# Kernel tuning notes

Hardware: AMD Instinct MI355X
Metric: run time of the kernel (lower is better)

## Reference

```python
import jax, jax.numpy as jnp
import numpy as np

N_NODES = 50000
N_EDGES = 800000
N_FEAT = 128
DIM = 64
N_GRAPHS = 512


def setup_inputs() -> dict:
    key = jax.random.key(0)
    k1, k2, k3, k4, k5, k6 = jax.random.split(key, 6)
    x = jax.random.normal(k1, (N_NODES, N_FEAT), dtype=jnp.float32)
    edge_index = jax.random.randint(k2, (2, N_EDGES), 0, N_NODES, dtype=jnp.int64)
    batch = jnp.sort(jax.random.randint(k3, (N_NODES,), 0, N_GRAPHS, dtype=jnp.int64))
    W1 = jax.random.normal(k4, (N_FEAT, DIM), dtype=jnp.float32) * 0.05
    W2 = jax.random.normal(k5, (DIM, DIM), dtype=jnp.float32) * 0.05
    Wfc = jax.random.normal(k6, (DIM, 1), dtype=jnp.float32) * 0.05
    return {"x": x, "edge_index": edge_index, "batch": batch,
            "W1": W1, "W2": W2, "Wfc": Wfc}


def _gcn_conv(h, src, dst, W):
    # GCNConv(normalize=False, bias=False): linear transform then scatter-add
    # over edges: out[dst] += (h @ W)[src]
    h = jnp.einsum('nf,fd->nd', h, W)
    return jax.ops.segment_sum(h[src], dst, num_segments=N_NODES)


def reference(x, edge_index, batch, W1, W2, Wfc):
    src, dst = edge_index[0], edge_index[1]
    h = jax.nn.relu(_gcn_conv(x, src, dst, W1))          # [N, DIM]
    h = _gcn_conv(h, src, dst, W2)                        # [N, DIM]
    # global_mean_pool over graph ids
    counts = jax.ops.segment_sum(jnp.ones((N_NODES,), h.dtype), batch,
                                 num_segments=N_GRAPHS)   # [G]
    pooled = jax.ops.segment_sum(h, batch, num_segments=N_GRAPHS)
    pooled = pooled / jnp.maximum(counts, 1.0)[:, None]   # [G, DIM]
    return jax.nn.sigmoid(pooled @ Wfc)                   # [G, 1]
```

## Files before the change

### kernel.cpp

```cpp
#include <hip/hip_runtime.h>
#include <cmath>

#define N_NODES 50000
#define N_EDGES 800000
#define N_FEAT 128
#define DIM 64
#define N_GRAPHS 512
#define GGRID ((N_NODES + 63) / 64)
#define NBKT GGRID
#define BH_BLK 128
#define EPB (N_EDGES / BH_BLK)
#define NCNT (NBKT * BH_BLK)
#define P2_NBLK ((NCNT + 511) / 512)
#define BKT_CAP 2048

__device__ __forceinline__ unsigned short f2bf(float f) {
  union { float f; unsigned int u; } v; v.f = f;
  return (unsigned short)((v.u + 0x7FFFu + ((v.u >> 16) & 1u)) >> 16);
}
__device__ __forceinline__ float bf2f(unsigned short u) {
  union { unsigned int u; float f; } v; v.u = (unsigned int)u << 16;
  return v.f;
}

__global__ __launch_bounds__(256) void bhist_w2fc(const int* __restrict__ dst,
                                                  int* __restrict__ cnt,
                                                  const float* __restrict__ W2,
                                                  const float* __restrict__ Wfc,
                                                  float* __restrict__ w2fc) {
  if (blockIdx.x == BH_BLK) {
    int k = threadIdx.x;
    if (k < 64) {
      float s = 0.f;
#pragma unroll 8
      for (int j = 0; j < 64; j++) s += W2[k * 64 + j] * Wfc[j];
      w2fc[k] = s;
    }
    return;
  }
  __shared__ int lh[NBKT];
  const int tid = threadIdx.x, k = blockIdx.x;
  for (int i = tid; i < NBKT; i += 256) lh[i] = 0;
  __syncthreads();
  const int base = k * EPB;
  for (int j = tid; j < EPB; j += 256)
    atomicAdd(&lh[dst[base + j] >> 6], 1);
  __syncthreads();
  for (int i = tid; i < NBKT; i += 256) cnt[i * BH_BLK + k] = lh[i];
}

__global__ __launch_bounds__(256) void f_psum(const int* __restrict__ cnt,
                                              int* __restrict__ partials) {
  __shared__ int ws[4];
  const int tid = threadIdx.x;
  const int2* cnt2 = (const int2*)cnt;
  int idx = blockIdx.x * 256 + tid;
  int v = 0;
  if (idx * 2 < NCNT) { int2 c = cnt2[idx]; v = c.x + c.y; }
#pragma unroll
  for (int off = 32; off; off >>= 1) v += __shfl_down(v, off, 64);
  int lane = tid & 63, w = tid >> 6;
  if (lane == 0) ws[w] = v;
  __syncthreads();
  if (tid == 0) partials[blockIdx.x] = ws[0] + ws[1] + ws[2] + ws[3];
}

__global__ __launch_bounds__(256) void f_sblocks(int* __restrict__ cnt,
                                                 const int* __restrict__ partials,
                                                 int* __restrict__ bucket_ptr) {
  __shared__ int buf[256];
  __shared__ int pbuf[256];
  const int tid = threadIdx.x;
  int2* cnt2 = (int2*)cnt;
  const int idx = blockIdx.x * 256 + tid;
  int2 c = make_int2(0, 0);
  if (idx * 2 < NCNT) c = cnt2[idx];
  int s = c.x + c.y;
  buf[tid] = s;
  pbuf[tid] = (tid < P2_NBLK) ? partials[tid] : 0;
  __syncthreads();
  for (int off = 1; off < 256; off <<= 1) {
    int t1 = (tid >= off) ? buf[tid - off] : 0;
    int t2 = (tid >= off) ? pbuf[tid - off] : 0;
    __syncthreads();
    buf[tid] += t1;
    pbuf[tid] += t2;
    __syncthreads();
  }
  const int thr_excl = buf[tid] - s;
  const int base = (blockIdx.x > 0) ? pbuf[blockIdx.x - 1] : 0;
  if (idx * 2 < NCNT) {
    int e0 = base + thr_excl;
    cnt2[idx] = make_int2(e0, e0 + c.x);
    int p = idx * 2;
    if ((p & (BH_BLK - 1)) == 0) bucket_ptr[p >> 7] = e0;
    if (p + 1 == NCNT - 1) bucket_ptr[NBKT] = e0 + c.x + c.y;
  }
}

template<int K>
__device__ __forceinline__ void gemm_body_bf(const float* __restrict__ A,
                                             const float* __restrict__ W,
                                             unsigned short* __restrict__ out,
                                             int M, int row0, int tid,
                                             float* sX, float* sW) {
  const int tx = tid & 15, ty = tid >> 4;
  const int q = tid & 7, r0 = tid >> 3;
  float acc[4][4] = {};

  for (int kb = 0; kb < K; kb += 32) {
    __syncthreads();
    if ((kb & 63) == 0) {
#pragma unroll
      for (int i = 0; i < 16; i++)
        sW[i * 256 + tid] = W[kb * 64 + i * 256 + tid];
    }
#pragma unroll
    for (int rr = 0; rr < 64; rr += 32) {
      int r = r0 + rr;
      int gr = row0 + r;
      float4 v = make_float4(0.f, 0.f, 0.f, 0.f);
      if (gr < M) v = *(const float4*)&A[(size_t)gr * K + kb + q * 4];
      *(float4*)&sX[r * 36 + q * 4] = v;
    }
    __syncthreads();

    const int kw = kb & 63;
#pragma unroll 4
    for (int k = 0; k < 32; k += 4) {
      float4 wv[4];
#pragma unroll
      for (int kk = 0; kk < 4; kk++)
        wv[kk] = *(const float4*)&sW[(kw + k + kk) * 64 + tx * 4];
#pragma unroll
      for (int r = 0; r < 4; r++) {
        float4 xv = *(const float4*)&sX[(ty * 4 + r) * 36 + k];
        const float xs[4] = {xv.x, xv.y, xv.z, xv.w};
#pragma unroll
        for (int kk = 0; kk < 4; kk++) {
          acc[r][0] += xs[kk] * wv[kk].x;
          acc[r][1] += xs[kk] * wv[kk].y;
          acc[r][2] += xs[kk] * wv[kk].z;
          acc[r][3] += xs[kk] * wv[kk].w;
        }
      }
    }
  }

#pragma unroll
  for (int r = 0; r < 4; r++) {
    int gr = row0 + ty * 4 + r;
    if (gr < M) {
      ushort4 u;
      u.x = f2bf(acc[r][0]); u.y = f2bf(acc[r][1]);
      u.z = f2bf(acc[r][2]); u.w = f2bf(acc[r][3]);
      *(ushort4*)&out[(size_t)gr * 64 + tx * 4] = u;
    }
  }
}

__global__ __launch_bounds__(256) void gemm1_bscatter(
    const float* __restrict__ x, const float* __restrict__ W1,
    unsigned short* __restrict__ h1, const int* __restrict__ src,
    const int* __restrict__ dst, const int* __restrict__ cnt,
    unsigned int* __restrict__ ebuf) {
  __shared__ float sX[64 * 36];
  __shared__ float sW[64 * 64];
  const int tid = threadIdx.x;
  if (blockIdx.x < GGRID) {
    gemm_body_bf<N_FEAT>(x, W1, h1, N_NODES, blockIdx.x * 64, tid, sX, sW);
  } else {
    int* loff = (int*)sX;
    const int k = blockIdx.x - GGRID;
    for (int i = tid; i < NBKT; i += 256) loff[i] = cnt[i * BH_BLK + k];
    __syncthreads();
    const int base = k * EPB;
    for (int j = tid; j < EPB; j += 256) {
      int e = base + j;
      int d = dst[e];
      int pos = atomicAdd(&loff[d >> 6], 1);
      ebuf[pos] = ((unsigned int)src[e] << 6) | (unsigned int)(d & 63);
    }
  }
}

__global__ __launch_bounds__(1024, 8) void gather_z_fused(
    const unsigned short* __restrict__ h1,
    const unsigned int* __restrict__ ebuf,
    const int* __restrict__ bucket_ptr,
    const float* __restrict__ w2fc,
    float* __restrict__ z) {
  __shared__ int colL[BKT_CAP];
  __shared__ int lstart[64];
  __shared__ int lcur[64];
  __shared__ float sw[64];
  const int tid = threadIdx.x;
  const int b = blockIdx.x;
  const int p0 = bucket_ptr[b];
  int cnt = bucket_ptr[b + 1] - p0;
  if (cnt > BKT_CAP) cnt = BKT_CAP;

  if (tid < 64) { lstart[tid] = 0; sw[tid] = w2fc[tid]; }
  __syncthreads();
  for (int i = tid; i < cnt; i += 1024)
    atomicAdd(&lstart[ebuf[p0 + i] & 63], 1);
  __syncthreads();
  if (tid < 64) {
    int v = lstart[tid], s = v;
#pragma unroll
    for (int off = 1; off < 64; off <<= 1) {
      int t = __shfl_up(s, off, 64);
      if (tid >= off) s += t;
    }
    lstart[tid] = s - v;
    lcur[tid] = s - v;
  }
  __syncthreads();
  for (int i = tid; i < cnt; i += 1024) {
    unsigned int u = ebuf[p0 + i];
    int pos = atomicAdd(&lcur[u & 63], 1);
    colL[pos] = (int)(u >> 6);
  }
  __syncthreads();

  const int lane = tid & 63, w = tid >> 6;
  const int eo = lane >> 4, qfo = (lane & 15) << 2;
#pragma unroll
  for (int ni = 0; ni < 4; ni++) {
    const int r = ni * 16 + w;
    const int i1 = lcur[r];
    int i = lstart[r];
    float4 acc = make_float4(0.f, 0.f, 0.f, 0.f);
    for (; i + 16 <= i1; i += 16) {
      int s0 = colL[i + eo];
      int s1 = colL[i + 4 + eo];
      int s2 = colL[i + 8 + eo];
      int s3 = colL[i + 12 + eo];
      ushort4 u0 = *(const ushort4*)&h1[(size_t)s0 * 64 + qfo];
      ushort4 u1 = *(const ushort4*)&h1[(size_t)s1 * 64 + qfo];
      ushort4 u2 = *(const ushort4*)&h1[(size_t)s2 * 64 + qfo];
      ushort4 u3 = *(const ushort4*)&h1[(size_t)s3 * 64 + qfo];
      acc.x += (bf2f(u0.x) + bf2f(u1.x)) + (bf2f(u2.x) + bf2f(u3.x));
      acc.y += (bf2f(u0.y) + bf2f(u1.y)) + (bf2f(u2.y) + bf2f(u3.y));
      acc.z += (bf2f(u0.z) + bf2f(u1.z)) + (bf2f(u2.z) + bf2f(u3.z));
      acc.w += (bf2f(u0.w) + bf2f(u1.w)) + (bf2f(u2.w) + bf2f(u3.w));
    }
    for (; i + 4 <= i1; i += 4) {
      int s = colL[i + eo];
      ushort4 u = *(const ushort4*)&h1[(size_t)s * 64 + qfo];
      acc.x += bf2f(u.x); acc.y += bf2f(u.y);
      acc.z += bf2f(u.z); acc.w += bf2f(u.w);
    }
    if (eo < i1 - i) {
      int s = colL[i + eo];
      ushort4 u = *(const ushort4*)&h1[(size_t)s * 64 + qfo];
      acc.x += bf2f(u.x); acc.y += bf2f(u.y);
      acc.z += bf2f(u.z); acc.w += bf2f(u.w);
    }
#pragma unroll
    for (int m = 16; m <= 32; m <<= 1) {
      acc.x += __shfl_xor(acc.x, m, 64);
      acc.y += __shfl_xor(acc.y, m, 64);
      acc.z += __shfl_xor(acc.z, m, 64);
      acc.w += __shfl_xor(acc.w, m, 64);
    }
    float p = fmaxf(acc.x, 0.f) * sw[qfo] + fmaxf(acc.y, 0.f) * sw[qfo + 1] +
              fmaxf(acc.z, 0.f) * sw[qfo + 2] + fmaxf(acc.w, 0.f) * sw[qfo + 3];
#pragma unroll
    for (int m = 1; m <= 8; m <<= 1) p += __shfl_xor(p, m, 64);
    int node = b * 64 + r;
    if (lane == 0 && node < N_NODES) z[node] = p;
  }
}

__global__ __launch_bounds__(256) void graph_pool(const float* __restrict__ z,
                                                  const unsigned int* __restrict__ ebuf,
                                                  const int* __restrict__ bucket_ptr,
                                                  const int* __restrict__ batch,
                                                  float* __restrict__ out) {
  __shared__ float sacc[4];
  int g = blockIdx.x;
  int tid = threadIdx.x, lane = tid & 63, w = tid >> 6;

  int lo = 0, hi = N_NODES;
  while (lo < hi) { int mid = (lo + hi) >> 1; if (batch[mid] < g) lo = mid + 1; else hi = mid; }
  const int start = lo;
  hi = N_NODES;
  while (lo < hi) { int mid = (lo + hi) >> 1; if (batch[mid] < g + 1) lo = mid + 1; else hi = mid; }
  const int end = lo;

  float s = 0.f;
  if (end > start) {
    const int b0 = start >> 6, b1 = ((end - 1) >> 6) + 1;
    for (int b = b0; b < b1; b++) {
      const int q0 = bucket_ptr[b], q1 = bucket_ptr[b + 1];
      const int base = b << 6;
      for (int i = q0 + tid; i < q1; i += 256) {
        unsigned int u = ebuf[i];
        int d = base + (int)(u & 63);
        if (d >= start && d < end) s += z[u >> 6];
      }
    }
  }
#pragma unroll
  for (int off = 32; off; off >>= 1) s += __shfl_down(s, off, 64);
  if (lane == 0) sacc[w] = s;
  __syncthreads();
  if (tid == 0) {
    float v = sacc[0] + sacc[1] + sacc[2] + sacc[3];
    v /= fmaxf((float)(end - start), 1.f);
    out[g] = 1.f / (1.f + expf(-v));
  }
}

extern "C" void kernel_launch(void* const* d_in, const int* in_sizes, int n_in,
                              void* d_out, int out_size, void* d_ws, size_t ws_size,
                              hipStream_t stream) {
  const float* x     = (const float*)d_in[0];
  const int*   ei    = (const int*)d_in[1];
  const int*   batch = (const int*)d_in[2];
  const float* W1    = (const float*)d_in[3];
  const float* W2    = (const float*)d_in[4];
  const float* Wfc   = (const float*)d_in[5];
  float*       out   = (float*)d_out;

  const int* src = ei;
  const int* dst = ei + N_EDGES;

  char* ws = (char*)d_ws;
  unsigned short* h1 = (unsigned short*)(ws);
  float* z    = (float*)(ws + (size_t)N_NODES * DIM * 2);
  float* w2fc = z + N_NODES;
  int*   cnt  = (int*)(w2fc + 64);
  int*   partials = cnt + NCNT;
  unsigned int* ebuf = (unsigned int*)(partials + P2_NBLK);
  int*   bucket_ptr  = (int*)(ebuf + N_EDGES);

  bhist_w2fc<<<BH_BLK + 1, 256, 0, stream>>>(dst, cnt, W2, Wfc, w2fc);
  f_psum<<<P2_NBLK, 256, 0, stream>>>(cnt, partials);
  f_sblocks<<<P2_NBLK, 256, 0, stream>>>(cnt, partials, bucket_ptr);

  gemm1_bscatter<<<GGRID + BH_BLK, 256, 0, stream>>>(x, W1, h1, src, dst, cnt, ebuf);

  gather_z_fused<<<NBKT, 1024, 0, stream>>>(h1, ebuf, bucket_ptr, w2fc, z);

  graph_pool<<<N_GRAPHS, 256, 0, stream>>>(z, ebuf, bucket_ptr, batch, out);
}
```

Before: 147.9 us.

## Use bf16 split-precision MFMA for first-layer GEMM with swizzled LDS

```diff
diff --git a/kernel.cpp b/kernel.cpp
--- a/kernel.cpp
+++ b/kernel.cpp
@@ -14,6 +14,9 @@
 #define P2_NBLK ((NCNT + 511) / 512)
 #define BKT_CAP 2048
 
+typedef short short8 __attribute__((ext_vector_type(8)));
+typedef float floatx4 __attribute__((ext_vector_type(4)));
+
 __device__ __forceinline__ unsigned short f2bf(float f) {
   union { float f; unsigned int u; } v; v.f = f;
   return (unsigned short)((v.u + 0x7FFFu + ((v.u >> 16) & 1u)) >> 16);
@@ -27,7 +30,10 @@
                                                   int* __restrict__ cnt,
                                                   const float* __restrict__ W2,
                                                   const float* __restrict__ Wfc,
-                                                  float* __restrict__ w2fc) {
+                                                  float* __restrict__ w2fc,
+                                                  const float* __restrict__ W1,
+                                                  unsigned short* __restrict__ w1sh,
+                                                  unsigned short* __restrict__ w1sl) {
   if (blockIdx.x == BH_BLK) {
     int k = threadIdx.x;
     if (k < 64) {
@@ -35,6 +41,21 @@
 #pragma unroll 8
       for (int j = 0; j < 64; j++) s += W2[k * 64 + j] * Wfc[j];
       w2fc[k] = s;
+    }
+    return;
+  }
+  if (blockIdx.x == BH_BLK + 1) {
+    int tid = threadIdx.x;
+#pragma unroll
+    for (int i = 0; i < 32; i++) {
+      int idx = i * 256 + tid;
+      int kk = idx & 127, c = idx >> 7;
+      float f = W1[kk * 64 + c];
+      unsigned short h = f2bf(f);
+      unsigned short l = f2bf(f - bf2f(h));
+      int didx = c * 128 + (kk ^ ((c & 15) << 3));
+      w1sh[didx] = h;
+      w1sl[didx] = l;
     }
     return;
   }
@@ -98,79 +119,92 @@
   }
 }
 
-template<int K>
-__device__ __forceinline__ void gemm_body_bf(const float* __restrict__ A,
-                                             const float* __restrict__ W,
-                                             unsigned short* __restrict__ out,
-                                             int M, int row0, int tid,
-                                             float* sX, float* sW) {
-  const int tx = tid & 15, ty = tid >> 4;
-  const int q = tid & 7, r0 = tid >> 3;
-  float acc[4][4] = {};
-
-  for (int kb = 0; kb < K; kb += 32) {
-    __syncthreads();
-    if ((kb & 63) == 0) {
-#pragma unroll
-      for (int i = 0; i < 16; i++)
-        sW[i * 256 + tid] = W[kb * 64 + i * 256 + tid];
-    }
-#pragma unroll
-    for (int rr = 0; rr < 64; rr += 32) {
-      int r = r0 + rr;
-      int gr = row0 + r;
-      float4 v = make_float4(0.f, 0.f, 0.f, 0.f);
-      if (gr < M) v = *(const float4*)&A[(size_t)gr * K + kb + q * 4];
-      *(float4*)&sX[r * 36 + q * 4] = v;
-    }
-    __syncthreads();
-
-    const int kw = kb & 63;
-#pragma unroll 4
-    for (int k = 0; k < 32; k += 4) {
-      float4 wv[4];
-#pragma unroll
-      for (int kk = 0; kk < 4; kk++)
-        wv[kk] = *(const float4*)&sW[(kw + k + kk) * 64 + tx * 4];
-#pragma unroll
-      for (int r = 0; r < 4; r++) {
-        float4 xv = *(const float4*)&sX[(ty * 4 + r) * 36 + k];
-        const float xs[4] = {xv.x, xv.y, xv.z, xv.w};
-#pragma unroll
-        for (int kk = 0; kk < 4; kk++) {
-          acc[r][0] += xs[kk] * wv[kk].x;
-          acc[r][1] += xs[kk] * wv[kk].y;
-          acc[r][2] += xs[kk] * wv[kk].z;
-          acc[r][3] += xs[kk] * wv[kk].w;
-        }
-      }
-    }
-  }
-
-#pragma unroll
-  for (int r = 0; r < 4; r++) {
-    int gr = row0 + ty * 4 + r;
-    if (gr < M) {
-      ushort4 u;
-      u.x = f2bf(acc[r][0]); u.y = f2bf(acc[r][1]);
-      u.z = f2bf(acc[r][2]); u.w = f2bf(acc[r][3]);
-      *(ushort4*)&out[(size_t)gr * 64 + tx * 4] = u;
+__device__ __forceinline__ void gemm1_mfma(const float* __restrict__ x,
+                                           const unsigned short* __restrict__ w1sh,
+                                           const unsigned short* __restrict__ w1sl,
+                                           unsigned short* __restrict__ h1,
+                                           int row0, int tid,
+                                           unsigned short* sXh, unsigned short* sXl,
+                                           unsigned short* sWh, unsigned short* sWl) {
+  const int4* wh4 = (const int4*)w1sh;
+  const int4* wl4 = (const int4*)w1sl;
+  int4* sWh4 = (int4*)sWh;
+  int4* sWl4 = (int4*)sWl;
+#pragma unroll
+  for (int i = 0; i < 4; i++) {
+    sWh4[i * 256 + tid] = wh4[i * 256 + tid];
+    sWl4[i * 256 + tid] = wl4[i * 256 + tid];
+  }
+#pragma unroll
+  for (int i = 0; i < 8; i++) {
+    int fid = i * 256 + tid;
+    int r = fid >> 5;
+    int c4 = (fid & 31) << 2;
+    int gr = row0 + r;
+    float4 v = make_float4(0.f, 0.f, 0.f, 0.f);
+    if (gr < N_NODES) v = *(const float4*)&x[(size_t)gr * N_FEAT + c4];
+    ushort4 h, l;
+    h.x = f2bf(v.x); l.x = f2bf(v.x - bf2f(h.x));
+    h.y = f2bf(v.y); l.y = f2bf(v.y - bf2f(h.y));
+    h.z = f2bf(v.z); l.z = f2bf(v.z - bf2f(h.z));
+    h.w = f2bf(v.w); l.w = f2bf(v.w - bf2f(h.w));
+    int idx = r * 128 + (c4 ^ ((r & 15) << 3));
+    *(ushort4*)&sXh[idx] = h;
+    *(ushort4*)&sXl[idx] = l;
+  }
+  __syncthreads();
+
+  const int lane = tid & 63, w = tid >> 6;
+  const int g = lane >> 4, c15 = lane & 15;
+  const int ra = (w << 4) + c15;
+  const int akey = c15 << 3;
+  floatx4 acc[4];
+#pragma unroll
+  for (int i = 0; i < 4; i++) acc[i] = (floatx4){0.f, 0.f, 0.f, 0.f};
+
+#pragma unroll
+  for (int kb = 0; kb < 128; kb += 32) {
+    const int ka = kb + g * 8;
+    short8 ah = *(const short8*)&sXh[ra * 128 + (ka ^ akey)];
+    short8 al = *(const short8*)&sXl[ra * 128 + (ka ^ akey)];
+#pragma unroll
+    for (int ct = 0; ct < 4; ct++) {
+      const int cb = ct * 16 + c15;
+      const int bi = cb * 128 + (ka ^ akey);
+      short8 bh = *(const short8*)&sWh[bi];
+      short8 bl = *(const short8*)&sWl[bi];
+      acc[ct] = __builtin_amdgcn_mfma_f32_16x16x32_bf16(ah, bh, acc[ct], 0, 0, 0);
+      acc[ct] = __builtin_amdgcn_mfma_f32_16x16x32_bf16(ah, bl, acc[ct], 0, 0, 0);
+      acc[ct] = __builtin_amdgcn_mfma_f32_16x16x32_bf16(al, bh, acc[ct], 0, 0, 0);
+    }
+  }
+
+#pragma unroll
+  for (int ct = 0; ct < 4; ct++) {
+#pragma unroll
+    for (int r = 0; r < 4; r++) {
+      int gr = row0 + (w << 4) + (g << 2) + r;
+      if (gr < N_NODES) h1[(size_t)gr * 64 + ct * 16 + c15] = f2bf(acc[ct][r]);
     }
   }
 }
 
 __global__ __launch_bounds__(256) void gemm1_bscatter(
-    const float* __restrict__ x, const float* __restrict__ W1,
+    const float* __restrict__ x,
+    const unsigned short* __restrict__ w1sh,
+    const unsigned short* __restrict__ w1sl,
     unsigned short* __restrict__ h1, const int* __restrict__ src,
     const int* __restrict__ dst, const int* __restrict__ cnt,
     unsigned int* __restrict__ ebuf) {
-  __shared__ float sX[64 * 36];
-  __shared__ float sW[64 * 64];
+  __shared__ __align__(16) unsigned short sXh[64 * 128];
+  __shared__ __align__(16) unsigned short sXl[64 * 128];
+  __shared__ __align__(16) unsigned short sWh[64 * 128];
+  __shared__ __align__(16) unsigned short sWl[64 * 128];
   const int tid = threadIdx.x;
   if (blockIdx.x < GGRID) {
-    gemm_body_bf<N_FEAT>(x, W1, h1, N_NODES, blockIdx.x * 64, tid, sX, sW);
+    gemm1_mfma(x, w1sh, w1sl, h1, blockIdx.x * 64, tid, sXh, sXl, sWh, sWl);
   } else {
-    int* loff = (int*)sX;
+    int* loff = (int*)sXh;
     const int k = blockIdx.x - GGRID;
     for (int i = tid; i < NBKT; i += 256) loff[i] = cnt[i * BH_BLK + k];
     __syncthreads();
@@ -329,18 +363,22 @@
 
   char* ws = (char*)d_ws;
   unsigned short* h1 = (unsigned short*)(ws);
-  float* z    = (float*)(ws + (size_t)N_NODES * DIM * 2);
+  unsigned short* w1sh = (unsigned short*)(ws + (size_t)N_NODES * DIM * 2);
+  unsigned short* w1sl = w1sh + N_FEAT * DIM;
+  float* z    = (float*)(w1sl + N_FEAT * DIM);
   float* w2fc = z + N_NODES;
   int*   cnt  = (int*)(w2fc + 64);
   int*   partials = cnt + NCNT;
   unsigned int* ebuf = (unsigned int*)(partials + P2_NBLK);
   int*   bucket_ptr  = (int*)(ebuf + N_EDGES);
 
-  bhist_w2fc<<<BH_BLK + 1, 256, 0, stream>>>(dst, cnt, W2, Wfc, w2fc);
+  bhist_w2fc<<<BH_BLK + 2, 256, 0, stream>>>(dst, cnt, W2, Wfc, w2fc,
+                                             W1, w1sh, w1sl);
   f_psum<<<P2_NBLK, 256, 0, stream>>>(cnt, partials);
   f_sblocks<<<P2_NBLK, 256, 0, stream>>>(cnt, partials, bucket_ptr);
 
-  gemm1_bscatter<<<GGRID + BH_BLK, 256, 0, stream>>>(x, W1, h1, src, dst, cnt, ebuf);
+  gemm1_bscatter<<<GGRID + BH_BLK, 256, 0, stream>>>(x, w1sh, w1sl, h1, src,
+                                                     dst, cnt, ebuf);
 
   gather_z_fused<<<NBKT, 1024, 0, stream>>>(h1, ebuf, bucket_ptr, w2fc, z);
 
```

Result: slower. 151.8 us (+2.6%).
